# Performance work log

Measured on AMD Instinct MI355X. Metric: run time of the kernel, lower is better.

## Reference

```python
import jax, jax.numpy as jnp
import numpy as np

EPS = 1e-12  # torch F.normalize eps


def setup_inputs() -> dict:
    key = jax.random.key(0)
    k1, k2, k3 = jax.random.split(key, 3)
    b, c, h, w = 4, 192, 128, 128
    num_heads = 8
    in1 = jax.random.normal(k1, (b, c, h, w), dtype=jnp.float32)
    in2 = jax.random.normal(k2, (b, c, h, w), dtype=jnp.float32)
    scale = jnp.ones((num_heads, 1, 1), dtype=jnp.float32)
    proj_w = jax.random.normal(k3, (c, c), dtype=jnp.float32) * (1.0 / np.sqrt(c))
    return {"in1": in1, "in2": in2, "scale": scale, "proj_w": proj_w, "num_heads": num_heads}


def reference(in1, in2, scale, proj_w, num_heads):
    b, c, h, w = in1.shape
    hd = c // num_heads
    hw = h * w
    # b (head c) h w -> b head c (h w)
    q = in1.reshape(b, num_heads, hd, hw)
    k = in2.reshape(b, num_heads, hd, hw)
    # L2-normalize along the (h w) axis, torch eps semantics
    q = q / jnp.maximum(jnp.linalg.norm(q, axis=-1, keepdims=True), EPS)
    k = k / jnp.maximum(jnp.linalg.norm(k, axis=-1, keepdims=True), EPS)
    # channel-wise attention: [b, head, c, c]
    attn = jnp.einsum('bhcn,bhdn->bhcd', q, k) * scale  # scale broadcasts [head,1,1]
    attn = jax.nn.softmax(attn, axis=-1)
    out = jnp.einsum('bhcd,bhdn->bhcn', attn, k)
    out = out.reshape(b, c, h, w)
    # 1x1 conv projection (no bias)
    out = jnp.einsum('oc,bchw->bohw', proj_w, out)
    return out
```

## Files before the change

kernel.cpp:

```cpp
#include <hip/hip_runtime.h>
#include <hip/hip_bf16.h>
#include <math.h>

#define BATCH 4
#define NHEAD 8
#define HD 24
#define CH 192
#define HW 16384
#define SPL 64
#define SROW 640

#define OFF_MO (32 * SPL * SROW)

#define LSTR 132

typedef __attribute__((ext_vector_type(8)))  short bf16x8;
typedef __attribute__((ext_vector_type(16))) float f32x16;

__device__ __forceinline__ unsigned short bf16rne(float x) {
    union { float f; unsigned u; } v; v.f = x;
    unsigned u = v.u;
    return (unsigned short)((u + 0x7FFFu + ((u >> 16) & 1u)) >> 16);
}

__device__ __forceinline__ unsigned pack2(float a, float b) {
    union { __hip_bfloat162 h; unsigned u; } c;
    c.h = __float22bfloat162_rn(float2{a, b});
    return c.u;
}

__global__ __launch_bounds__(256, 4) void kA(const float* __restrict__ q,
                                             const float* __restrict__ k,
                                             float* __restrict__ ws) {
    __shared__ unsigned int tile[2][HD * LSTR];

    const int bh   = blockIdx.x;
    const int ch   = blockIdx.y;
    const int t    = threadIdx.x;
    const int lane = t & 63;
    const int wave = t >> 6;
    const int m    = lane & 31;
    const int hi   = lane >> 5;

    const float* qb = q + (size_t)bh * HD * HW + ch * 256;
    const float* kb = k + (size_t)bh * HD * HW + ch * 256;

    #pragma unroll
    for (int j = 0; j < 6; ++j) {
        const int idx = j * 256 + t;
        const int row = idx >> 6;
        const int c64 = idx & 63;
        float4 qv = *(const float4*)(qb + (size_t)row * HW + c64 * 4);
        float4 kv = *(const float4*)(kb + (size_t)row * HW + c64 * 4);
        *(uint2*)&tile[0][row * LSTR + c64 * 2] = make_uint2(pack2(qv.x, qv.y), pack2(qv.z, qv.w));
        *(uint2*)&tile[1][row * LSTR + c64 * 2] = make_uint2(pack2(kv.x, kv.y), pack2(kv.z, kv.w));
    }
    __syncthreads();

    const int rowc = (m < HD) ? m : 0;
    f32x16 aQK = {}, aQQ = {}, aKK = {};
    #pragma unroll
    for (int s = 0; s < 4; ++s) {
        const int off = (wave * 64 + s * 16) >> 1;
        bf16x8 aq = *(const bf16x8*)&tile[0][rowc * LSTR + off + hi * 4];
        bf16x8 bk = *(const bf16x8*)&tile[1][rowc * LSTR + off + hi * 4];
        aQK = __builtin_amdgcn_mfma_f32_32x32x16_bf16(aq, bk, aQK, 0, 0, 0);
        aQQ = __builtin_amdgcn_mfma_f32_32x32x16_bf16(aq, aq, aQQ, 0, 0, 0);
        aKK = __builtin_amdgcn_mfma_f32_32x32x16_bf16(bk, bk, aKK, 0, 0, 0);
    }
    __syncthreads();

    float* red = (float*)tile;
    if (m < HD) {
        #pragma unroll
        for (int r = 0; r < 16; ++r) {
            const int i = (r & 3) + 8 * (r >> 2) + 4 * hi;
            if (i < HD) {
                red[wave * 624 + i * HD + m] = aQK[r];
                if (i == m) {
                    red[wave * 624 + 576 + i] = aQQ[r];
                    red[wave * 624 + 600 + i] = aKK[r];
                }
            }
        }
    }
    __syncthreads();

    float* Srow = ws + ((size_t)bh * SPL + ch) * SROW;
    for (int e = t; e < 624; e += 256)
        Srow[e] = red[e] + red[624 + e] + red[1248 + e] + red[1872 + e];
}

__global__ __launch_bounds__(1024) void kB(const float* __restrict__ scale,
                                           const float* __restrict__ w,
                                           float* __restrict__ ws,
                                           unsigned short* __restrict__ Mo) {
    const int bh = blockIdx.x;
    const int b  = bh >> 3;
    const int h  = bh & 7;
    const int t  = threadIdx.x;
    const int g  = t >> 8;
    const int u  = t & 255;

    __shared__ float part[4][624];
    __shared__ float SA[624];
    __shared__ float qinv[HD], kinv[HD];
    __shared__ float wl[CH * HD];

    const float* base = ws + (size_t)bh * SPL * SROW;

    float a0 = 0.f, a1 = 0.f, a2 = 0.f;
    for (int sp = g * 16; sp < g * 16 + 16; ++sp) {
        const float* r = base + (size_t)sp * SROW;
        a0 += r[u];
        a1 += r[u + 256];
        if (u < 112) a2 += r[u + 512];
    }
    part[g][u] = a0;
    part[g][u + 256] = a1;
    if (u < 112) part[g][u + 512] = a2;

    for (int idx = t; idx < CH * HD; idx += 1024) {
        int o = idx / HD, dd = idx % HD;
        wl[idx] = w[o * CH + h * HD + dd];
    }
    __syncthreads();

    if (t < 624) SA[t] = part[0][t] + part[1][t] + part[2][t] + part[3][t];
    __syncthreads();

    if (t < 2 * HD) {
        float inv = 1.0f / fmaxf(sqrtf(SA[576 + t]), 1e-12f);
        if (t < HD) qinv[t] = inv; else kinv[t - HD] = inv;
    }
    __syncthreads();

    const float sc = scale[h];
    if (t < 576) SA[t] = SA[t] * qinv[t / HD] * kinv[t % HD] * sc;
    __syncthreads();

    if (t < HD) {
        float m = -1e30f;
        for (int j = 0; j < HD; ++j) m = fmaxf(m, SA[t * HD + j]);
        float sum = 0.f;
        for (int j = 0; j < HD; ++j) {
            float v = expf(SA[t * HD + j] - m);
            SA[t * HD + j] = v;
            sum += v;
        }
        float r = 1.0f / sum;
        for (int j = 0; j < HD; ++j) SA[t * HD + j] *= r;
    }
    __syncthreads();

    for (int idx = t; idx < CH * HD; idx += 1024) {
        int o = idx / HD, j = idx % HD;
        float v = 0.f;
        #pragma unroll
        for (int i = 0; i < HD; ++i) v = fmaf(wl[o * HD + i], SA[i * HD + j], v);
        Mo[(size_t)b * CH * CH + (size_t)o * CH + h * HD + j] = bf16rne(v * kinv[j]);
    }
}

#define KCN 64
#define CSTEP 64
#define BSTR2 36

__global__ __launch_bounds__(256, 4) void kC(const float* __restrict__ k,
                                             const unsigned short* __restrict__ Mo,
                                             float* __restrict__ out) {
    __shared__ unsigned int Bt[KCN * BSTR2];

    const int t    = threadIdx.x;
    const int lane = t & 63;
    const int wave = t >> 6;
    const int n31  = lane & 31;
    const int hi   = lane >> 5;
    const int nt   = wave & 1;
    const int otb  = (wave >> 1) * 3;

    const int nb = blockIdx.x * KCN;
    const int b  = blockIdx.y;

    const float* kb = k + (size_t)b * CH * HW;
    const unsigned short* Mob = Mo + (size_t)b * CH * CH;

    const int np = t & 31;
    const int cg = t >> 5;

    f32x16 acc[3] = {};

    for (int c0 = 0; c0 < CH; c0 += CSTEP) {
        if (c0) __syncthreads();
        float2 v[8];
        #pragma unroll
        for (int cc = 0; cc < 8; ++cc)
            v[cc] = *(const float2*)(kb + (size_t)(c0 + cg * 8 + cc) * HW + nb + np * 2);
        unsigned int w0[4], w1[4];
        #pragma unroll
        for (int g = 0; g < 4; ++g) {
            w0[g] = pack2(v[2 * g].x, v[2 * g + 1].x);
            w1[g] = pack2(v[2 * g].y, v[2 * g + 1].y);
        }
        const int n0 = np * 2;
        *(uint2*)&Bt[n0 * BSTR2 + cg * 4]           = make_uint2(w0[0], w0[1]);
        *(uint2*)&Bt[n0 * BSTR2 + cg * 4 + 2]       = make_uint2(w0[2], w0[3]);
        *(uint2*)&Bt[(n0 + 1) * BSTR2 + cg * 4]     = make_uint2(w1[0], w1[1]);
        *(uint2*)&Bt[(n0 + 1) * BSTR2 + cg * 4 + 2] = make_uint2(w1[2], w1[3]);
        __syncthreads();

        #pragma unroll
        for (int kc = 0; kc < 4; ++kc) {
            bf16x8 Bf = *(const bf16x8*)&Bt[(nt * 32 + n31) * BSTR2 + kc * 8 + hi * 4];
            #pragma unroll
            for (int oi = 0; oi < 3; ++oi) {
                const unsigned short* ap =
                    Mob + (size_t)((otb + oi) * 32 + n31) * CH + c0 + kc * 16 + hi * 8;
                bf16x8 Af = *(const bf16x8*)ap;
                acc[oi] = __builtin_amdgcn_mfma_f32_32x32x16_bf16(Af, Bf, acc[oi], 0, 0, 0);
            }
        }
    }

    float* op = out + (size_t)b * CH * HW;
    const int n = nb + nt * 32 + n31;
    #pragma unroll
    for (int oi = 0; oi < 3; ++oi)
        #pragma unroll
        for (int r = 0; r < 16; ++r) {
            int o = (otb + oi) * 32 + (r & 3) + 8 * (r >> 2) + 4 * hi;
            op[(size_t)o * HW + n] = acc[oi][r];
        }
}

extern "C" void kernel_launch(void* const* d_in, const int* in_sizes, int n_in,
                              void* d_out, int out_size, void* d_ws, size_t ws_size,
                              hipStream_t stream) {
    const float* in1   = (const float*)d_in[0];
    const float* in2   = (const float*)d_in[1];
    const float* scale = (const float*)d_in[2];
    const float* projw = (const float*)d_in[3];
    float* ws  = (float*)d_ws;
    float* out = (float*)d_out;
    unsigned short* Mo = (unsigned short*)(ws + OFF_MO);

    kA<<<dim3(32, SPL), 256, 0, stream>>>(in1, in2, ws);
    kB<<<32, 1024, 0, stream>>>(scale, projw, ws, Mo);
    kC<<<dim3(HW / KCN, BATCH), 256, 0, stream>>>(in2, Mo, out);
}
```

Measured before the change: 174.9 us.

## Halve kA split count and stage full K tile in kC with float4 loads

kA now walks two 256-column halves per block, which halves the number of partial Gram rows (SPL 64→32) written to the workspace and summed in kB. kC loads the full 192-channel K tile for its 64 columns into LDS in one pass using float4 loads, replacing the three-step loop with its repeated barriers. The goals are fewer blocks and less workspace reduction in kA/kB, plus more memory-level parallelism and fewer syncs in kC. In exchange, kC uses more LDS per block, which may limit occupancy, and kA has less parallelism.

```diff
diff --git a/kernel.cpp b/kernel.cpp
--- a/kernel.cpp
+++ b/kernel.cpp
@@ -7,7 +7,7 @@
 #define HD 24
 #define CH 192
 #define HW 16384
-#define SPL 64
+#define SPL 32
 #define SROW 640
 
 #define OFF_MO (32 * SPL * SROW)
@@ -41,34 +41,40 @@
     const int wave = t >> 6;
     const int m    = lane & 31;
     const int hi   = lane >> 5;
-
-    const float* qb = q + (size_t)bh * HD * HW + ch * 256;
-    const float* kb = k + (size_t)bh * HD * HW + ch * 256;
-
-    #pragma unroll
-    for (int j = 0; j < 6; ++j) {
-        const int idx = j * 256 + t;
-        const int row = idx >> 6;
-        const int c64 = idx & 63;
-        float4 qv = *(const float4*)(qb + (size_t)row * HW + c64 * 4);
-        float4 kv = *(const float4*)(kb + (size_t)row * HW + c64 * 4);
-        *(uint2*)&tile[0][row * LSTR + c64 * 2] = make_uint2(pack2(qv.x, qv.y), pack2(qv.z, qv.w));
-        *(uint2*)&tile[1][row * LSTR + c64 * 2] = make_uint2(pack2(kv.x, kv.y), pack2(kv.z, kv.w));
-    }
-    __syncthreads();
-
     const int rowc = (m < HD) ? m : 0;
+
     f32x16 aQK = {}, aQQ = {}, aKK = {};
-    #pragma unroll
-    for (int s = 0; s < 4; ++s) {
-        const int off = (wave * 64 + s * 16) >> 1;
-        bf16x8 aq = *(const bf16x8*)&tile[0][rowc * LSTR + off + hi * 4];
-        bf16x8 bk = *(const bf16x8*)&tile[1][rowc * LSTR + off + hi * 4];
-        aQK = __builtin_amdgcn_mfma_f32_32x32x16_bf16(aq, bk, aQK, 0, 0, 0);
-        aQQ = __builtin_amdgcn_mfma_f32_32x32x16_bf16(aq, aq, aQQ, 0, 0, 0);
-        aKK = __builtin_amdgcn_mfma_f32_32x32x16_bf16(bk, bk, aKK, 0, 0, 0);
-    }
-    __syncthreads();
+
+    #pragma unroll
+    for (int half = 0; half < 2; ++half) {
+        const float* qb = q + (size_t)bh * HD * HW + ch * 512 + half * 256;
+        const float* kb = k + (size_t)bh * HD * HW + ch * 512 + half * 256;
+
+        #pragma unroll
+        for (int j = 0; j < 6; ++j) {
+            const int idx = j * 256 + t;
+            const int row = idx >> 6;
+            const int c64 = idx & 63;
+            float4 qv = *(const float4*)(qb + (size_t)row * HW + c64 * 4);
+            float4 kv = *(const float4*)(kb + (size_t)row * HW + c64 * 4);
+            *(uint2*)&tile[0][row * LSTR + c64 * 2] =
+                make_uint2(pack2(qv.x, qv.y), pack2(qv.z, qv.w));
+            *(uint2*)&tile[1][row * LSTR + c64 * 2] =
+                make_uint2(pack2(kv.x, kv.y), pack2(kv.z, kv.w));
+        }
+        __syncthreads();
+
+        #pragma unroll
+        for (int s = 0; s < 4; ++s) {
+            const int off = (wave * 64 + s * 16) >> 1;
+            bf16x8 aq = *(const bf16x8*)&tile[0][rowc * LSTR + off + hi * 4];
+            bf16x8 bk = *(const bf16x8*)&tile[1][rowc * LSTR + off + hi * 4];
+            aQK = __builtin_amdgcn_mfma_f32_32x32x16_bf16(aq, bk, aQK, 0, 0, 0);
+            aQQ = __builtin_amdgcn_mfma_f32_32x32x16_bf16(aq, aq, aQQ, 0, 0, 0);
+            aKK = __builtin_amdgcn_mfma_f32_32x32x16_bf16(bk, bk, aKK, 0, 0, 0);
+        }
+        __syncthreads();
+    }
 
     float* red = (float*)tile;
     if (m < HD) {
@@ -110,7 +116,7 @@
     const float* base = ws + (size_t)bh * SPL * SROW;
 
     float a0 = 0.f, a1 = 0.f, a2 = 0.f;
-    for (int sp = g * 16; sp < g * 16 + 16; ++sp) {
+    for (int sp = g * 8; sp < g * 8 + 8; ++sp) {
         const float* r = base + (size_t)sp * SROW;
         a0 += r[u];
         a1 += r[u + 256];
@@ -163,13 +169,12 @@
 }
 
 #define KCN 64
-#define CSTEP 64
-#define BSTR2 36
+#define BSTR3 100
 
 __global__ __launch_bounds__(256, 4) void kC(const float* __restrict__ k,
                                              const unsigned short* __restrict__ Mo,
                                              float* __restrict__ out) {
-    __shared__ unsigned int Bt[KCN * BSTR2];
+    __shared__ unsigned int Bt[KCN * BSTR3];
 
     const int t    = threadIdx.x;
     const int lane = t & 63;
@@ -185,40 +190,35 @@
     const float* kb = k + (size_t)b * CH * HW;
     const unsigned short* Mob = Mo + (size_t)b * CH * CH;
 
-    const int np = t & 31;
-    const int cg = t >> 5;
+    const int np4 = t & 15;
+    const int cg4 = t >> 4;
+
+    #pragma unroll
+    for (int s = 0; s < 3; ++s) {
+        float4 v[4];
+        #pragma unroll
+        for (int cc = 0; cc < 4; ++cc)
+            v[cc] = *(const float4*)(kb + (size_t)(s * 64 + cg4 * 4 + cc) * HW + nb + np4 * 4);
+        #pragma unroll
+        for (int r = 0; r < 4; ++r) {
+            float x0 = (&v[0].x)[r], x1 = (&v[1].x)[r];
+            float x2 = (&v[2].x)[r], x3 = (&v[3].x)[r];
+            *(uint2*)&Bt[(np4 * 4 + r) * BSTR3 + s * 32 + cg4 * 2] =
+                make_uint2(pack2(x0, x1), pack2(x2, x3));
+        }
+    }
+    __syncthreads();
 
     f32x16 acc[3] = {};
-
-    for (int c0 = 0; c0 < CH; c0 += CSTEP) {
-        if (c0) __syncthreads();
-        float2 v[8];
-        #pragma unroll
-        for (int cc = 0; cc < 8; ++cc)
-            v[cc] = *(const float2*)(kb + (size_t)(c0 + cg * 8 + cc) * HW + nb + np * 2);
-        unsigned int w0[4], w1[4];
-        #pragma unroll
-        for (int g = 0; g < 4; ++g) {
-            w0[g] = pack2(v[2 * g].x, v[2 * g + 1].x);
-            w1[g] = pack2(v[2 * g].y, v[2 * g + 1].y);
-        }
-        const int n0 = np * 2;
-        *(uint2*)&Bt[n0 * BSTR2 + cg * 4]           = make_uint2(w0[0], w0[1]);
-        *(uint2*)&Bt[n0 * BSTR2 + cg * 4 + 2]       = make_uint2(w0[2], w0[3]);
-        *(uint2*)&Bt[(n0 + 1) * BSTR2 + cg * 4]     = make_uint2(w1[0], w1[1]);
-        *(uint2*)&Bt[(n0 + 1) * BSTR2 + cg * 4 + 2] = make_uint2(w1[2], w1[3]);
-        __syncthreads();
-
-        #pragma unroll
-        for (int kc = 0; kc < 4; ++kc) {
-            bf16x8 Bf = *(const bf16x8*)&Bt[(nt * 32 + n31) * BSTR2 + kc * 8 + hi * 4];
-            #pragma unroll
-            for (int oi = 0; oi < 3; ++oi) {
-                const unsigned short* ap =
-                    Mob + (size_t)((otb + oi) * 32 + n31) * CH + c0 + kc * 16 + hi * 8;
-                bf16x8 Af = *(const bf16x8*)ap;
-                acc[oi] = __builtin_amdgcn_mfma_f32_32x32x16_bf16(Af, Bf, acc[oi], 0, 0, 0);
-            }
+    #pragma unroll
+    for (int kc = 0; kc < 12; ++kc) {
+        bf16x8 Bf = *(const bf16x8*)&Bt[(nt * 32 + n31) * BSTR3 + kc * 8 + hi * 4];
+        #pragma unroll
+        for (int oi = 0; oi < 3; ++oi) {
+            const unsigned short* ap =
+                Mob + (size_t)((otb + oi) * 32 + n31) * CH + kc * 16 + hi * 8;
+            bf16x8 Af = *(const bf16x8*)ap;
+            acc[oi] = __builtin_amdgcn_mfma_f32_32x32x16_bf16(Af, Bf, acc[oi], 0, 0, 0);
         }
     }
 
```

Result: no change. 175.4 us (+0.3%).
